# Optimization experiments

Hardware: AMD Instinct MI355X
Metric: run time of the kernel (lower is better)

Reference implementation:

```python
import jax, jax.numpy as jnp
import numpy as np

N = 50000        # nodes
F_IN = 128       # input features
HID = 128        # hidden_size
H = 4            # heads
C = HID // H     # per-head channels (32)
E_RAND = 800000  # random edges; + N self loops -> E = 850000
NEG_SLOPE = 0.2  # PyG GATConv default leaky_relu slope


def setup_inputs() -> dict:
    key = jax.random.key(0)
    ks = jax.random.split(key, 12)
    x = jax.random.normal(ks[0], (N, F_IN), jnp.float32)
    src_r = jax.random.randint(ks[1], (E_RAND,), 0, N)
    dst_r = jax.random.randint(ks[2], (E_RAND,), 0, N)
    loops = jnp.arange(N)
    src = jnp.concatenate([src_r, loops]).astype(jnp.int32)
    dst = jnp.concatenate([dst_r, loops]).astype(jnp.int32)

    def glorot(k, shape):
        fan_in, fan_out = shape[0], shape[-1]
        lim = np.sqrt(6.0 / (fan_in + fan_out)).astype(np.float32)
        return jax.random.uniform(k, shape, jnp.float32, -lim, lim)

    return {
        "x": x, "src": src, "dst": dst,
        "W0": glorot(ks[3], (F_IN, HID)),
        "a_src0": glorot(ks[4], (H, C)),
        "a_dst0": glorot(ks[5], (H, C)),
        "b0": jnp.zeros((HID,), jnp.float32),
        "W1": glorot(ks[6], (HID, HID)),
        "a_src1": glorot(ks[7], (H, C)),
        "a_dst1": glorot(ks[8], (H, C)),
        "b1": jnp.zeros((HID,), jnp.float32),
    }


def gat_layer(x, W, a_src, a_dst, b, src, dst):
    # linear projection -> [N, H, C]
    xp = (x @ W).reshape(-1, H, C)
    # per-node attention logits [N, H]
    al_src = jnp.einsum("nhc,hc->nh", xp, a_src)
    al_dst = jnp.einsum("nhc,hc->nh", xp, a_dst)
    # edge logits [E, H]
    e = jax.nn.leaky_relu(al_src[src] + al_dst[dst], NEG_SLOPE)
    # scatter softmax over incoming edges of each destination node
    m = jax.ops.segment_max(e, dst, num_segments=N)
    p = jnp.exp(e - m[dst])
    s = jax.ops.segment_sum(p, dst, num_segments=N)
    alpha = p / (s[dst] + 1e-16)
    # weighted message aggregation: [E, H, C] scatter-add -> [N, H, C]
    out = jax.ops.segment_sum(xp[src] * alpha[:, :, None], dst, num_segments=N)
    return out.reshape(-1, H * C) + b  # concat heads + bias


def reference(x, src, dst, W0, a_src0, a_dst0, b0, W1, a_src1, a_dst1, b1):
    h = jax.nn.relu(gat_layer(x, W0, a_src0, a_dst0, b0, src, dst))
    h = jax.nn.relu(gat_layer(h, W1, a_src1, a_dst1, b1, src, dst))
    return h
```

## Files before the change

### kernel.cpp

```cpp
#include <hip/hip_runtime.h>
#include <math.h>

#define NEG_SLOPE 0.2f
#define BCAP 4096
#define TILE 4096

using short8 = __attribute__((ext_vector_type(8))) short;
using f32x4 = __attribute__((ext_vector_type(4))) float;

__device__ __forceinline__ float leaky(float x) { return x > 0.f ? x : NEG_SLOPE * x; }

__device__ __forceinline__ float wmax64(float v) {
#pragma unroll
  for (int off = 32; off; off >>= 1) v = fmaxf(v, __shfl_xor(v, off));
  return v;
}
__device__ __forceinline__ float wsum64(float v) {
#pragma unroll
  for (int off = 32; off; off >>= 1) v += __shfl_xor(v, off);
  return v;
}

__device__ __forceinline__ unsigned short f2bf(float f) {
  union { float f; unsigned u; } x; x.f = f;
  unsigned r = x.u + 0x7fff + ((x.u >> 16) & 1);
  return (unsigned short)(r >> 16);
}
__device__ __forceinline__ float bf2f(unsigned short h) {
  union { unsigned u; float f; } x; x.u = (unsigned)h << 16;
  return x.f;
}

__device__ __forceinline__ void acc8(float* a, float p, uint4 rv) {
  a[0] += p * __uint_as_float(rv.x << 16);
  a[1] += p * __uint_as_float(rv.x & 0xffff0000u);
  a[2] += p * __uint_as_float(rv.y << 16);
  a[3] += p * __uint_as_float(rv.y & 0xffff0000u);
  a[4] += p * __uint_as_float(rv.z << 16);
  a[5] += p * __uint_as_float(rv.z & 0xffff0000u);
  a[6] += p * __uint_as_float(rv.w << 16);
  a[7] += p * __uint_as_float(rv.w & 0xffff0000u);
}

__global__ __launch_bounds__(256) void k_hist_wsplit(
    const int* __restrict__ dst, int* __restrict__ blkhist, int E, int nb, int nblk,
    const float* __restrict__ W0, const float* __restrict__ W1,
    unsigned short* __restrict__ Wth0, unsigned short* __restrict__ Wtl0,
    unsigned short* __restrict__ Wth1, unsigned short* __restrict__ Wtl1) {
  __shared__ int h[512];
  if (blockIdx.x < 128) {
    int i = blockIdx.x * 256 + threadIdx.x;
    int j = i & 16383;
    int k = j >> 7, n = j & 127;
    const float* W = (i < 16384) ? W0 : W1;
    float v = W[j];
    unsigned short hi = f2bf(v);
    unsigned short lo = f2bf(v - bf2f(hi));
    if (i < 16384) {
      Wth0[n * 128 + k] = hi;
      Wtl0[n * 128 + k] = lo;
    } else {
      Wth1[n * 128 + k] = hi;
      Wtl1[n * 128 + k] = lo;
    }
    return;
  }
  int blk = blockIdx.x - 128;
  for (int i = threadIdx.x; i < nb; i += 256) h[i] = 0;
  __syncthreads();
  int t0 = blk * TILE;
  int end = t0 + TILE < E ? t0 + TILE : E;
  for (int i = t0 + threadIdx.x; i < end; i += 256) atomicAdd(&h[dst[i] >> 7], 1);
  __syncthreads();
  for (int i = threadIdx.x; i < nb; i += 256) blkhist[(size_t)i * nblk + blk] = h[i];
}

__global__ __launch_bounds__(256) void k_bofs(int* __restrict__ blkhist,
                                              int* __restrict__ btot, int nblk) {
  __shared__ int sd[256];
  int b = blockIdx.x, t = threadIdx.x;
  int v = (t < nblk) ? blkhist[(size_t)b * nblk + t] : 0;
  sd[t] = v;
  __syncthreads();
  for (int off = 1; off < 256; off <<= 1) {
    int add = (t >= off) ? sd[t - off] : 0;
    __syncthreads();
    sd[t] += add;
    __syncthreads();
  }
  if (t < nblk) blkhist[(size_t)b * nblk + t] = sd[t] - v;
  if (t == 255) btot[b] = sd[255];
}

__global__ __launch_bounds__(256) void k_scatter2(
    const int* __restrict__ src, const int* __restrict__ dst,
    const int* __restrict__ blkhist, const int* __restrict__ btot,
    int2* __restrict__ bstore, int E, int nb, int nblk) {
  __shared__ int sd[256];
  __shared__ int bb[512];
  __shared__ int cur[512];
  int t = threadIdx.x, blk = blockIdx.x;
  int v0 = (2 * t < nb) ? btot[2 * t] : 0;
  int v1 = (2 * t + 1 < nb) ? btot[2 * t + 1] : 0;
  int s = v0 + v1;
  sd[t] = s;
  __syncthreads();
  for (int off = 1; off < 256; off <<= 1) {
    int add = (t >= off) ? sd[t - off] : 0;
    __syncthreads();
    sd[t] += add;
    __syncthreads();
  }
  int run = sd[t] - s;
  if (2 * t < nb) bb[2 * t] = run;
  if (2 * t + 1 < nb) bb[2 * t + 1] = run + v0;
  __syncthreads();
  for (int i = t; i < nb; i += 256)
    cur[i] = bb[i] + blkhist[(size_t)i * nblk + blk];
  __syncthreads();
  int t0 = blk * TILE;
  int end = t0 + TILE < E ? t0 + TILE : E;
  for (int i = t0 + t; i < end; i += 256) {
    int d = dst[i];
    int pos = atomicAdd(&cur[d >> 7], 1);
    bstore[pos] = make_int2(src[i], d);
  }
}

__global__ __launch_bounds__(256) void k_build(
    const int2* __restrict__ bstore, const int* __restrict__ btot,
    int* __restrict__ ssrc, int* __restrict__ deg, int* __restrict__ rstart, int N) {
  __shared__ int ls[BCAP];
  __shared__ unsigned char lloc[BCAP];
  __shared__ int lout[BCAP];
  __shared__ int hist[128];
  __shared__ int sc[128];
  __shared__ int lcur[128];
  __shared__ int red[256];
  int b = blockIdx.x;
  int t = threadIdx.x;
  int pacc = 0;
  for (int j = t; j < b; j += 256) pacc += btot[j];
  red[t] = pacc;
  __syncthreads();
  for (int off = 128; off; off >>= 1) {
    if (t < off) red[t] += red[t + off];
    __syncthreads();
  }
  int base = red[0];
  int cnt = btot[b];
  if (cnt > BCAP) cnt = BCAP;
  int nlo = b << 7;
  if (t < 128) { hist[t] = 0; lcur[t] = 0; }
  __syncthreads();
  for (int i = t; i < cnt; i += 256) {
    int2 e = bstore[base + i];
    int loc = e.y - nlo;
    ls[i] = e.x;
    lloc[i] = (unsigned char)loc;
    atomicAdd(&hist[loc], 1);
  }
  __syncthreads();
  int hv = (t < 128) ? hist[t] : 0;
  if (t < 128) sc[t] = hv;
  __syncthreads();
  for (int off = 1; off < 128; off <<= 1) {
    int add = (t < 128 && t >= off) ? sc[t - off] : 0;
    __syncthreads();
    if (t < 128) sc[t] += add;
    __syncthreads();
  }
  int lstart = (t < 128) ? sc[t] - hv : 0;
  if (t < 128) sc[t] = lstart;
  if (t < 128 && nlo + t < N) {
    deg[nlo + t] = hv;
    rstart[nlo + t] = base + lstart;
  }
  __syncthreads();
  for (int i = t; i < cnt; i += 256) {
    int loc = lloc[i];
    int slot = sc[loc] + atomicAdd(&lcur[loc], 1);
    lout[slot] = ls[i];
  }
  __syncthreads();
  for (int i = t; i < cnt; i += 256) ssrc[base + i] = lout[i];
}

#define PA 136
#define PW 40
__global__ __launch_bounds__(256, 2) void k_gemm_mfma(
    const float* __restrict__ A, const unsigned short* __restrict__ Wth,
    const unsigned short* __restrict__ Wtl, const float* __restrict__ a_src,
    const float* __restrict__ a_dst, unsigned short* __restrict__ xph,
    float* __restrict__ als, float* __restrict__ ald, int nrows) {
  __shared__ unsigned short Ah[64 * PA];
  __shared__ unsigned short Al[64 * PA];
  __shared__ unsigned short Wh[128 * PW];
  __shared__ unsigned short Wl[128 * PW];
  int t = threadIdx.x;
  int row0 = blockIdx.x * 64;

  const float4* A4 = (const float4*)A;
#pragma unroll
  for (int p = 0; p < 8; ++p) {
    int idx = t + p * 256;
    int row = idx >> 5, k4 = idx & 31;
    int gr = row0 + row;
    float4 v = make_float4(0.f, 0.f, 0.f, 0.f);
    if (gr < nrows) v = A4[(size_t)gr * 32 + k4];
    ushort4 hi, lo;
    hi.x = f2bf(v.x); lo.x = f2bf(v.x - bf2f(hi.x));
    hi.y = f2bf(v.y); lo.y = f2bf(v.y - bf2f(hi.y));
    hi.z = f2bf(v.z); lo.z = f2bf(v.z - bf2f(hi.z));
    hi.w = f2bf(v.w); lo.w = f2bf(v.w - bf2f(hi.w));
    *(ushort4*)&Ah[row * PA + k4 * 4] = hi;
    *(ushort4*)&Al[row * PA + k4 * 4] = lo;
  }

  int lane = t & 63, wv = t >> 6;
  int wr = wv >> 1, wc = wv & 1;
  int ml = lane & 15, q = lane >> 4;
  f32x4 acc[2][4] = {};

  for (int kb = 0; kb < 4; ++kb) {
    __syncthreads();
    int k0 = kb * 32;
#pragma unroll
    for (int p = 0; p < 8; ++p) {
      int idx = t + p * 256;
      int n = idx >> 4, kp = idx & 15;
      *(unsigned*)&Wh[n * PW + kp * 2] =
          *(const unsigned*)(Wth + (size_t)n * 128 + k0 + kp * 2);
      *(unsigned*)&Wl[n * PW + kp * 2] =
          *(const unsigned*)(Wtl + (size_t)n * 128 + k0 + kp * 2);
    }
    __syncthreads();
    int kf = k0 + q * 8;
    short8 a_h0 = *(const short8*)&Ah[(wr * 32 + ml) * PA + kf];
    short8 a_h1 = *(const short8*)&Ah[(wr * 32 + 16 + ml) * PA + kf];
    short8 a_l0 = *(const short8*)&Al[(wr * 32 + ml) * PA + kf];
    short8 a_l1 = *(const short8*)&Al[(wr * 32 + 16 + ml) * PA + kf];
#pragma unroll
    for (int ct = 0; ct < 4; ++ct) {
      int nb = (wc * 64 + ct * 16 + ml) * PW + q * 8;
      short8 b_h = *(const short8*)&Wh[nb];
      short8 b_l = *(const short8*)&Wl[nb];
      acc[0][ct] = __builtin_amdgcn_mfma_f32_16x16x32_bf16(a_h0, b_h, acc[0][ct], 0, 0, 0);
      acc[0][ct] = __builtin_amdgcn_mfma_f32_16x16x32_bf16(a_h0, b_l, acc[0][ct], 0, 0, 0);
      acc[0][ct] = __builtin_amdgcn_mfma_f32_16x16x32_bf16(a_l0, b_h, acc[0][ct], 0, 0, 0);
      acc[1][ct] = __builtin_amdgcn_mfma_f32_16x16x32_bf16(a_h1, b_h, acc[1][ct], 0, 0, 0);
      acc[1][ct] = __builtin_amdgcn_mfma_f32_16x16x32_bf16(a_h1, b_l, acc[1][ct], 0, 0, 0);
      acc[1][ct] = __builtin_amdgcn_mfma_f32_16x16x32_bf16(a_l1, b_h, acc[1][ct], 0, 0, 0);
    }
  }

  float asr[4], adr[4];
#pragma unroll
  for (int ct = 0; ct < 4; ++ct) {
    int col = (wc * 2 + (ct >> 1)) * 32 + (ct & 1) * 16 + ml;
    asr[ct] = a_src[col];
    adr[ct] = a_dst[col];
  }

#pragma unroll
  for (int rt = 0; rt < 2; ++rt) {
#pragma unroll
    for (int r = 0; r < 4; ++r) {
      int gr = row0 + wr * 32 + rt * 16 + q * 4 + r;
      bool valid = gr < nrows;
      if (valid) {
#pragma unroll
        for (int ct = 0; ct < 4; ++ct) {
          int gc = wc * 64 + ct * 16 + ml;
          xph[(size_t)gr * 128 + gc] = f2bf(acc[rt][ct][r]);
        }
      }
      float p0 = acc[rt][0][r] * asr[0] + acc[rt][1][r] * asr[1];
      float p1 = acc[rt][2][r] * asr[2] + acc[rt][3][r] * asr[3];
      float d0 = acc[rt][0][r] * adr[0] + acc[rt][1][r] * adr[1];
      float d1 = acc[rt][2][r] * adr[2] + acc[rt][3][r] * adr[3];
#pragma unroll
      for (int off = 1; off <= 8; off <<= 1) {
        p0 += __shfl_xor(p0, off); p1 += __shfl_xor(p1, off);
        d0 += __shfl_xor(d0, off); d1 += __shfl_xor(d1, off);
      }
      if (ml == 0 && valid) {
        als[(size_t)gr * 4 + wc * 2] = p0;
        als[(size_t)gr * 4 + wc * 2 + 1] = p1;
        ald[(size_t)gr * 4 + wc * 2] = d0;
        ald[(size_t)gr * 4 + wc * 2 + 1] = d1;
      }
    }
  }
}

__global__ __launch_bounds__(256) void k_aggregate(
    const unsigned short* __restrict__ xph, const float* __restrict__ als,
    const float* __restrict__ ald, const int* __restrict__ rstart,
    const int* __restrict__ deg, const int* __restrict__ ssrc,
    const float* __restrict__ bias, float* __restrict__ out, int N) {
  __shared__ float pbuf[4][128 * 4];
  __shared__ int snbuf[4][128];
  int wv = threadIdx.x >> 6;
  int lane = threadIdx.x & 63;
  int n = (blockIdx.x * blockDim.x + threadIdx.x) >> 6;
  if (n >= N) return;
  int start = rstart[n];
  int d = deg[n];
  float4 adv = *(const float4*)(ald + (size_t)n * 4);

  float m0, m1, m2, m3;
  float s0 = 0.f, s1 = 0.f, s2 = 0.f, s3 = 0.f;
  if (d <= 64) {
    int i = lane;
    bool valid = i < d;
    int sn = valid ? ssrc[start + i] : 0;
    if (valid) snbuf[wv][i] = sn;
    float4 av = *(const float4*)(als + (size_t)sn * 4);
    float L0 = valid ? leaky(av.x + adv.x) : -INFINITY;
    float L1 = valid ? leaky(av.y + adv.y) : -INFINITY;
    float L2 = valid ? leaky(av.z + adv.z) : -INFINITY;
    float L3 = valid ? leaky(av.w + adv.w) : -INFINITY;
    m0 = wmax64(L0); m1 = wmax64(L1); m2 = wmax64(L2); m3 = wmax64(L3);
    float p0 = __expf(L0 - m0);
    float p1 = __expf(L1 - m1);
    float p2 = __expf(L2 - m2);
    float p3 = __expf(L3 - m3);
    *(float4*)&pbuf[wv][lane * 4] = make_float4(p0, p1, p2, p3);
    s0 = wsum64(p0); s1 = wsum64(p1); s2 = wsum64(p2); s3 = wsum64(p3);
  } else {
    m0 = m1 = m2 = m3 = -INFINITY;
    for (int base = 0; base < d; base += 64) {
      int i = base + lane;
      bool valid = i < d;
      int sn = valid ? ssrc[start + i] : 0;
      if (valid) snbuf[wv][i] = sn;
      float4 av = *(const float4*)(als + (size_t)sn * 4);
      float L0 = valid ? leaky(av.x + adv.x) : -INFINITY;
      float L1 = valid ? leaky(av.y + adv.y) : -INFINITY;
      float L2 = valid ? leaky(av.z + adv.z) : -INFINITY;
      float L3 = valid ? leaky(av.w + adv.w) : -INFINITY;
      if (valid) *(float4*)&pbuf[wv][i * 4] = make_float4(L0, L1, L2, L3);
      m0 = fmaxf(m0, wmax64(L0)); m1 = fmaxf(m1, wmax64(L1));
      m2 = fmaxf(m2, wmax64(L2)); m3 = fmaxf(m3, wmax64(L3));
    }
    for (int base = 0; base < d; base += 64) {
      int i = base + lane;
      bool valid = i < d;
      float4 lv = valid ? *(const float4*)&pbuf[wv][i * 4]
                        : make_float4(-INFINITY, -INFINITY, -INFINITY, -INFINITY);
      float p0 = __expf(lv.x - m0), p1 = __expf(lv.y - m1);
      float p2 = __expf(lv.z - m2), p3 = __expf(lv.w - m3);
      if (valid) *(float4*)&pbuf[wv][i * 4] = make_float4(p0, p1, p2, p3);
      s0 += wsum64(p0); s1 += wsum64(p1); s2 += wsum64(p2); s3 += wsum64(p3);
    }
  }

  int cg = lane & 15;
  int es = lane >> 4;
  int c0 = cg * 8;
  int h = cg >> 2;
  float a[8] = {0.f, 0.f, 0.f, 0.f, 0.f, 0.f, 0.f, 0.f};
  int t = es;
  for (; t + 12 < d; t += 16) {
    int sn0 = snbuf[wv][t];
    int sn1 = snbuf[wv][t + 4];
    int sn2 = snbuf[wv][t + 8];
    int sn3 = snbuf[wv][t + 12];
    float q0 = pbuf[wv][t * 4 + h];
    float q1 = pbuf[wv][(t + 4) * 4 + h];
    float q2 = pbuf[wv][(t + 8) * 4 + h];
    float q3 = pbuf[wv][(t + 12) * 4 + h];
    uint4 r0 = *(const uint4*)(xph + (size_t)sn0 * 128 + c0);
    uint4 r1 = *(const uint4*)(xph + (size_t)sn1 * 128 + c0);
    uint4 r2 = *(const uint4*)(xph + (size_t)sn2 * 128 + c0);
    uint4 r3 = *(const uint4*)(xph + (size_t)sn3 * 128 + c0);
    acc8(a, q0, r0);
    acc8(a, q1, r1);
    acc8(a, q2, r2);
    acc8(a, q3, r3);
  }
  for (; t < d; t += 4) {
    int sn = snbuf[wv][t];
    float p = pbuf[wv][t * 4 + h];
    uint4 rv = *(const uint4*)(xph + (size_t)sn * 128 + c0);
    acc8(a, p, rv);
  }
#pragma unroll
  for (int off = 16; off <= 32; off <<= 1) {
#pragma unroll
    for (int j = 0; j < 8; ++j) a[j] += __shfl_xor(a[j], off);
  }
  if (es == 0) {
    float sden = h == 0 ? s0 : h == 1 ? s1 : h == 2 ? s2 : s3;
    float inv = 1.f / (sden + 1e-16f);
    float4 bv0 = *(const float4*)(bias + c0);
    float4 bv1 = *(const float4*)(bias + c0 + 4);
    float4 o0, o1;
    o0.x = fmaxf(a[0] * inv + bv0.x, 0.f);
    o0.y = fmaxf(a[1] * inv + bv0.y, 0.f);
    o0.z = fmaxf(a[2] * inv + bv0.z, 0.f);
    o0.w = fmaxf(a[3] * inv + bv0.w, 0.f);
    o1.x = fmaxf(a[4] * inv + bv1.x, 0.f);
    o1.y = fmaxf(a[5] * inv + bv1.y, 0.f);
    o1.z = fmaxf(a[6] * inv + bv1.z, 0.f);
    o1.w = fmaxf(a[7] * inv + bv1.w, 0.f);
    *(float4*)(out + (size_t)n * 128 + c0) = o0;
    *(float4*)(out + (size_t)n * 128 + c0 + 4) = o1;
  }
}

extern "C" void kernel_launch(void* const* d_in, const int* in_sizes, int n_in,
                              void* d_out, int out_size, void* d_ws, size_t ws_size,
                              hipStream_t stream) {
  const float* x   = (const float*)d_in[0];
  const int*   src = (const int*)d_in[1];
  const int*   dst = (const int*)d_in[2];
  const float* W0  = (const float*)d_in[3];
  const float* as0 = (const float*)d_in[4];
  const float* ad0 = (const float*)d_in[5];
  const float* b0  = (const float*)d_in[6];
  const float* W1  = (const float*)d_in[7];
  const float* as1 = (const float*)d_in[8];
  const float* ad1 = (const float*)d_in[9];
  const float* b1  = (const float*)d_in[10];
  float* out = (float*)d_out;

  int N = in_sizes[0] / 128;
  int E = in_sizes[1];
  int NB = (N + 127) >> 7;
  int NBLK = (E + TILE - 1) / TILE;

  char* w = (char*)d_ws;
  auto alloc = [&](size_t bytes) {
    char* p = w;
    w += (bytes + 255) & ~(size_t)255;
    return p;
  };
  int* deg     = (int*)alloc((size_t)N * 4);
  int* rstart  = (int*)alloc((size_t)N * 4);
  int* blkhist = (int*)alloc((size_t)NB * NBLK * 4);
  int* btot    = (int*)alloc((size_t)NB * 4);
  int2* bstore = (int2*)alloc((size_t)E * 8);
  int* ssrc    = (int*)alloc((size_t)E * 4);
  unsigned short* xph = (unsigned short*)alloc((size_t)N * 128 * 2);
  float* hbuf  = (float*)alloc((size_t)N * 128 * 4);
  float* als   = (float*)alloc((size_t)N * 4 * 4);
  float* ald   = (float*)alloc((size_t)N * 4 * 4);
  unsigned short* Wth0 = (unsigned short*)alloc(16384 * 2);
  unsigned short* Wtl0 = (unsigned short*)alloc(16384 * 2);
  unsigned short* Wth1 = (unsigned short*)alloc(16384 * 2);
  unsigned short* Wtl1 = (unsigned short*)alloc(16384 * 2);

  k_hist_wsplit<<<128 + NBLK, 256, 0, stream>>>(dst, blkhist, E, NB, NBLK,
                                                W0, W1, Wth0, Wtl0, Wth1, Wtl1);
  k_bofs<<<NB, 256, 0, stream>>>(blkhist, btot, NBLK);
  k_scatter2<<<NBLK, 256, 0, stream>>>(src, dst, blkhist, btot, bstore, E, NB, NBLK);
  k_build<<<NB, 256, 0, stream>>>(bstore, btot, ssrc, deg, rstart, N);

  int gb = (N + 63) / 64;
  k_gemm_mfma<<<gb, 256, 0, stream>>>(x, Wth0, Wtl0, as0, ad0, xph, als, ald, N);
  k_aggregate<<<(N + 3) / 4, 256, 0, stream>>>(xph, als, ald, rstart, deg, ssrc, b0, hbuf, N);

  k_gemm_mfma<<<gb, 256, 0, stream>>>(hbuf, Wth1, Wtl1, as1, ad1, xph, als, ald, N);
  k_aggregate<<<(N + 3) / 4, 256, 0, stream>>>(xph, als, ald, rstart, deg, ssrc, b1, out, N);
}
```

Measured before the change: 249.9 us.

## Fuse layer-0 GEMM into scatter kernel, pack bucket entries, simplify gather loop

Layer-0 GEMM blocks are appended to the scatter kernel's grid, so the projection runs alongside the edge bucketing and one launch is removed. Bucket entries are packed into a single int (local dst in the high 16 bits, src in the low 16), which halves the bucket store traffic. TILE doubles to 8192, halving the number of scatter blocks. The aggregation loop's manual 4-way unroll is replaced by a plain loop with unroll 2, giving up some memory-level parallelism in exchange for lower register pressure. The 16-bit src packing is only valid while N is at most 65536.

```diff
diff --git a/kernel.cpp b/kernel.cpp
--- a/kernel.cpp
+++ b/kernel.cpp
@@ -3,7 +3,7 @@
 
 #define NEG_SLOPE 0.2f
 #define BCAP 4096
-#define TILE 4096
+#define TILE 8192
 
 using short8 = __attribute__((ext_vector_type(8))) short;
 using f32x4 = __attribute__((ext_vector_type(4))) float;
@@ -40,6 +40,114 @@
   a[5] += p * __uint_as_float(rv.z & 0xffff0000u);
   a[6] += p * __uint_as_float(rv.w << 16);
   a[7] += p * __uint_as_float(rv.w & 0xffff0000u);
+}
+
+#define PA 136
+#define PW 40
+__device__ void gemm_body(
+    const float* __restrict__ A, const unsigned short* __restrict__ Wth,
+    const unsigned short* __restrict__ Wtl, const float* __restrict__ a_src,
+    const float* __restrict__ a_dst, unsigned short* __restrict__ xph,
+    float* __restrict__ als, float* __restrict__ ald, int nrows, int blk) {
+  __shared__ unsigned short Ah[64 * PA];
+  __shared__ unsigned short Al[64 * PA];
+  __shared__ unsigned short Wh[128 * PW];
+  __shared__ unsigned short Wl[128 * PW];
+  int t = threadIdx.x;
+  int row0 = blk * 64;
+
+  const float4* A4 = (const float4*)A;
+#pragma unroll
+  for (int p = 0; p < 8; ++p) {
+    int idx = t + p * 256;
+    int row = idx >> 5, k4 = idx & 31;
+    int gr = row0 + row;
+    float4 v = make_float4(0.f, 0.f, 0.f, 0.f);
+    if (gr < nrows) v = A4[(size_t)gr * 32 + k4];
+    ushort4 hi, lo;
+    hi.x = f2bf(v.x); lo.x = f2bf(v.x - bf2f(hi.x));
+    hi.y = f2bf(v.y); lo.y = f2bf(v.y - bf2f(hi.y));
+    hi.z = f2bf(v.z); lo.z = f2bf(v.z - bf2f(hi.z));
+    hi.w = f2bf(v.w); lo.w = f2bf(v.w - bf2f(hi.w));
+    *(ushort4*)&Ah[row * PA + k4 * 4] = hi;
+    *(ushort4*)&Al[row * PA + k4 * 4] = lo;
+  }
+
+  int lane = t & 63, wv = t >> 6;
+  int wr = wv >> 1, wc = wv & 1;
+  int ml = lane & 15, q = lane >> 4;
+  f32x4 acc[2][4] = {};
+
+  for (int kb = 0; kb < 4; ++kb) {
+    __syncthreads();
+    int k0 = kb * 32;
+#pragma unroll
+    for (int p = 0; p < 8; ++p) {
+      int idx = t + p * 256;
+      int n = idx >> 4, kp = idx & 15;
+      *(unsigned*)&Wh[n * PW + kp * 2] =
+          *(const unsigned*)(Wth + (size_t)n * 128 + k0 + kp * 2);
+      *(unsigned*)&Wl[n * PW + kp * 2] =
+          *(const unsigned*)(Wtl + (size_t)n * 128 + k0 + kp * 2);
+    }
+    __syncthreads();
+    int kf = k0 + q * 8;
+    short8 a_h0 = *(const short8*)&Ah[(wr * 32 + ml) * PA + kf];
+    short8 a_h1 = *(const short8*)&Ah[(wr * 32 + 16 + ml) * PA + kf];
+    short8 a_l0 = *(const short8*)&Al[(wr * 32 + ml) * PA + kf];
+    short8 a_l1 = *(const short8*)&Al[(wr * 32 + 16 + ml) * PA + kf];
+#pragma unroll
+    for (int ct = 0; ct < 4; ++ct) {
+      int nb = (wc * 64 + ct * 16 + ml) * PW + q * 8;
+      short8 b_h = *(const short8*)&Wh[nb];
+      short8 b_l = *(const short8*)&Wl[nb];
+      acc[0][ct] = __builtin_amdgcn_mfma_f32_16x16x32_bf16(a_h0, b_h, acc[0][ct], 0, 0, 0);
+      acc[0][ct] = __builtin_amdgcn_mfma_f32_16x16x32_bf16(a_h0, b_l, acc[0][ct], 0, 0, 0);
+      acc[0][ct] = __builtin_amdgcn_mfma_f32_16x16x32_bf16(a_l0, b_h, acc[0][ct], 0, 0, 0);
+      acc[1][ct] = __builtin_amdgcn_mfma_f32_16x16x32_bf16(a_h1, b_h, acc[1][ct], 0, 0, 0);
+      acc[1][ct] = __builtin_amdgcn_mfma_f32_16x16x32_bf16(a_h1, b_l, acc[1][ct], 0, 0, 0);
+      acc[1][ct] = __builtin_amdgcn_mfma_f32_16x16x32_bf16(a_l1, b_h, acc[1][ct], 0, 0, 0);
+    }
+  }
+
+  float asr[4], adr[4];
+#pragma unroll
+  for (int ct = 0; ct < 4; ++ct) {
+    int col = (wc * 2 + (ct >> 1)) * 32 + (ct & 1) * 16 + ml;
+    asr[ct] = a_src[col];
+    adr[ct] = a_dst[col];
+  }
+
+#pragma unroll
+  for (int rt = 0; rt < 2; ++rt) {
+#pragma unroll
+    for (int r = 0; r < 4; ++r) {
+      int gr = row0 + wr * 32 + rt * 16 + q * 4 + r;
+      bool valid = gr < nrows;
+      if (valid) {
+#pragma unroll
+        for (int ct = 0; ct < 4; ++ct) {
+          int gc = wc * 64 + ct * 16 + ml;
+          xph[(size_t)gr * 128 + gc] = f2bf(acc[rt][ct][r]);
+        }
+      }
+      float p0 = acc[rt][0][r] * asr[0] + acc[rt][1][r] * asr[1];
+      float p1 = acc[rt][2][r] * asr[2] + acc[rt][3][r] * asr[3];
+      float d0 = acc[rt][0][r] * adr[0] + acc[rt][1][r] * adr[1];
+      float d1 = acc[rt][2][r] * adr[2] + acc[rt][3][r] * adr[3];
+#pragma unroll
+      for (int off = 1; off <= 8; off <<= 1) {
+        p0 += __shfl_xor(p0, off); p1 += __shfl_xor(p1, off);
+        d0 += __shfl_xor(d0, off); d1 += __shfl_xor(d1, off);
+      }
+      if (ml == 0 && valid) {
+        als[(size_t)gr * 4 + wc * 2] = p0;
+        als[(size_t)gr * 4 + wc * 2 + 1] = p1;
+        ald[(size_t)gr * 4 + wc * 2] = d0;
+        ald[(size_t)gr * 4 + wc * 2 + 1] = d1;
+      }
+    }
+  }
 }
 
 __global__ __launch_bounds__(256) void k_hist_wsplit(
@@ -92,10 +200,18 @@
   if (t == 255) btot[b] = sd[255];
 }
 
-__global__ __launch_bounds__(256) void k_scatter2(
+__global__ __launch_bounds__(256, 2) void k_scatter2_gemm(
     const int* __restrict__ src, const int* __restrict__ dst,
     const int* __restrict__ blkhist, const int* __restrict__ btot,
-    int2* __restrict__ bstore, int E, int nb, int nblk) {
+    int* __restrict__ bstore, int E, int nb, int nblk,
+    const float* __restrict__ A, const unsigned short* __restrict__ Wth,
+    const unsigned short* __restrict__ Wtl, const float* __restrict__ a_src,
+    const float* __restrict__ a_dst, unsigned short* __restrict__ xph,
+    float* __restrict__ als, float* __restrict__ ald, int nrows) {
+  if ((int)blockIdx.x >= nblk) {
+    gemm_body(A, Wth, Wtl, a_src, a_dst, xph, als, ald, nrows, blockIdx.x - nblk);
+    return;
+  }
   __shared__ int sd[256];
   __shared__ int bb[512];
   __shared__ int cur[512];
@@ -123,12 +239,12 @@
   for (int i = t0 + t; i < end; i += 256) {
     int d = dst[i];
     int pos = atomicAdd(&cur[d >> 7], 1);
-    bstore[pos] = make_int2(src[i], d);
+    bstore[pos] = ((d & 127) << 16) | src[i];
   }
 }
 
 __global__ __launch_bounds__(256) void k_build(
-    const int2* __restrict__ bstore, const int* __restrict__ btot,
+    const int* __restrict__ bstore, const int* __restrict__ btot,
     int* __restrict__ ssrc, int* __restrict__ deg, int* __restrict__ rstart, int N) {
   __shared__ int ls[BCAP];
   __shared__ unsigned char lloc[BCAP];
@@ -154,9 +270,9 @@
   if (t < 128) { hist[t] = 0; lcur[t] = 0; }
   __syncthreads();
   for (int i = t; i < cnt; i += 256) {
-    int2 e = bstore[base + i];
-    int loc = e.y - nlo;
-    ls[i] = e.x;
+    int e = bstore[base + i];
+    int loc = e >> 16;
+    ls[i] = e & 0xffff;
     lloc[i] = (unsigned char)loc;
     atomicAdd(&hist[loc], 1);
   }
@@ -186,112 +302,12 @@
   for (int i = t; i < cnt; i += 256) ssrc[base + i] = lout[i];
 }
 
-#define PA 136
-#define PW 40
 __global__ __launch_bounds__(256, 2) void k_gemm_mfma(
     const float* __restrict__ A, const unsigned short* __restrict__ Wth,
     const unsigned short* __restrict__ Wtl, const float* __restrict__ a_src,
     const float* __restrict__ a_dst, unsigned short* __restrict__ xph,
     float* __restrict__ als, float* __restrict__ ald, int nrows) {
-  __shared__ unsigned short Ah[64 * PA];
-  __shared__ unsigned short Al[64 * PA];
-  __shared__ unsigned short Wh[128 * PW];
-  __shared__ unsigned short Wl[128 * PW];
-  int t = threadIdx.x;
-  int row0 = blockIdx.x * 64;
-
-  const float4* A4 = (const float4*)A;
-#pragma unroll
-  for (int p = 0; p < 8; ++p) {
-    int idx = t + p * 256;
-    int row = idx >> 5, k4 = idx & 31;
-    int gr = row0 + row;
-    float4 v = make_float4(0.f, 0.f, 0.f, 0.f);
-    if (gr < nrows) v = A4[(size_t)gr * 32 + k4];
-    ushort4 hi, lo;
-    hi.x = f2bf(v.x); lo.x = f2bf(v.x - bf2f(hi.x));
-    hi.y = f2bf(v.y); lo.y = f2bf(v.y - bf2f(hi.y));
-    hi.z = f2bf(v.z); lo.z = f2bf(v.z - bf2f(hi.z));
-    hi.w = f2bf(v.w); lo.w = f2bf(v.w - bf2f(hi.w));
-    *(ushort4*)&Ah[row * PA + k4 * 4] = hi;
-    *(ushort4*)&Al[row * PA + k4 * 4] = lo;
-  }
-
-  int lane = t & 63, wv = t >> 6;
-  int wr = wv >> 1, wc = wv & 1;
-  int ml = lane & 15, q = lane >> 4;
-  f32x4 acc[2][4] = {};
-
-  for (int kb = 0; kb < 4; ++kb) {
-    __syncthreads();
-    int k0 = kb * 32;
-#pragma unroll
-    for (int p = 0; p < 8; ++p) {
-      int idx = t + p * 256;
-      int n = idx >> 4, kp = idx & 15;
-      *(unsigned*)&Wh[n * PW + kp * 2] =
-          *(const unsigned*)(Wth + (size_t)n * 128 + k0 + kp * 2);
-      *(unsigned*)&Wl[n * PW + kp * 2] =
-          *(const unsigned*)(Wtl + (size_t)n * 128 + k0 + kp * 2);
-    }
-    __syncthreads();
-    int kf = k0 + q * 8;
-    short8 a_h0 = *(const short8*)&Ah[(wr * 32 + ml) * PA + kf];
-    short8 a_h1 = *(const short8*)&Ah[(wr * 32 + 16 + ml) * PA + kf];
-    short8 a_l0 = *(const short8*)&Al[(wr * 32 + ml) * PA + kf];
-    short8 a_l1 = *(const short8*)&Al[(wr * 32 + 16 + ml) * PA + kf];
-#pragma unroll
-    for (int ct = 0; ct < 4; ++ct) {
-      int nb = (wc * 64 + ct * 16 + ml) * PW + q * 8;
-      short8 b_h = *(const short8*)&Wh[nb];
-      short8 b_l = *(const short8*)&Wl[nb];
-      acc[0][ct] = __builtin_amdgcn_mfma_f32_16x16x32_bf16(a_h0, b_h, acc[0][ct], 0, 0, 0);
-      acc[0][ct] = __builtin_amdgcn_mfma_f32_16x16x32_bf16(a_h0, b_l, acc[0][ct], 0, 0, 0);
-      acc[0][ct] = __builtin_amdgcn_mfma_f32_16x16x32_bf16(a_l0, b_h, acc[0][ct], 0, 0, 0);
-      acc[1][ct] = __builtin_amdgcn_mfma_f32_16x16x32_bf16(a_h1, b_h, acc[1][ct], 0, 0, 0);
-      acc[1][ct] = __builtin_amdgcn_mfma_f32_16x16x32_bf16(a_h1, b_l, acc[1][ct], 0, 0, 0);
-      acc[1][ct] = __builtin_amdgcn_mfma_f32_16x16x32_bf16(a_l1, b_h, acc[1][ct], 0, 0, 0);
-    }
-  }
-
-  float asr[4], adr[4];
-#pragma unroll
-  for (int ct = 0; ct < 4; ++ct) {
-    int col = (wc * 2 + (ct >> 1)) * 32 + (ct & 1) * 16 + ml;
-    asr[ct] = a_src[col];
-    adr[ct] = a_dst[col];
-  }
-
-#pragma unroll
-  for (int rt = 0; rt < 2; ++rt) {
-#pragma unroll
-    for (int r = 0; r < 4; ++r) {
-      int gr = row0 + wr * 32 + rt * 16 + q * 4 + r;
-      bool valid = gr < nrows;
-      if (valid) {
-#pragma unroll
-        for (int ct = 0; ct < 4; ++ct) {
-          int gc = wc * 64 + ct * 16 + ml;
-          xph[(size_t)gr * 128 + gc] = f2bf(acc[rt][ct][r]);
-        }
-      }
-      float p0 = acc[rt][0][r] * asr[0] + acc[rt][1][r] * asr[1];
-      float p1 = acc[rt][2][r] * asr[2] + acc[rt][3][r] * asr[3];
-      float d0 = acc[rt][0][r] * adr[0] + acc[rt][1][r] * adr[1];
-      float d1 = acc[rt][2][r] * adr[2] + acc[rt][3][r] * adr[3];
-#pragma unroll
-      for (int off = 1; off <= 8; off <<= 1) {
-        p0 += __shfl_xor(p0, off); p1 += __shfl_xor(p1, off);
-        d0 += __shfl_xor(d0, off); d1 += __shfl_xor(d1, off);
-      }
-      if (ml == 0 && valid) {
-        als[(size_t)gr * 4 + wc * 2] = p0;
-        als[(size_t)gr * 4 + wc * 2 + 1] = p1;
-        ald[(size_t)gr * 4 + wc * 2] = d0;
-        ald[(size_t)gr * 4 + wc * 2 + 1] = d1;
-      }
-    }
-  }
+  gemm_body(A, Wth, Wtl, a_src, a_dst, xph, als, ald, nrows, blockIdx.x);
 }
 
 __global__ __launch_bounds__(256) void k_aggregate(
@@ -361,26 +377,8 @@
   int c0 = cg * 8;
   int h = cg >> 2;
   float a[8] = {0.f, 0.f, 0.f, 0.f, 0.f, 0.f, 0.f, 0.f};
-  int t = es;
-  for (; t + 12 < d; t += 16) {
-    int sn0 = snbuf[wv][t];
-    int sn1 = snbuf[wv][t + 4];
-    int sn2 = snbuf[wv][t + 8];
-    int sn3 = snbuf[wv][t + 12];
-    float q0 = pbuf[wv][t * 4 + h];
-    float q1 = pbuf[wv][(t + 4) * 4 + h];
-    float q2 = pbuf[wv][(t + 8) * 4 + h];
-    float q3 = pbuf[wv][(t + 12) * 4 + h];
-    uint4 r0 = *(const uint4*)(xph + (size_t)sn0 * 128 + c0);
-    uint4 r1 = *(const uint4*)(xph + (size_t)sn1 * 128 + c0);
-    uint4 r2 = *(const uint4*)(xph + (size_t)sn2 * 128 + c0);
-    uint4 r3 = *(const uint4*)(xph + (size_t)sn3 * 128 + c0);
-    acc8(a, q0, r0);
-    acc8(a, q1, r1);
-    acc8(a, q2, r2);
-    acc8(a, q3, r3);
-  }
-  for (; t < d; t += 4) {
+#pragma unroll 2
+  for (int t = es; t < d; t += 4) {
     int sn = snbuf[wv][t];
     float p = pbuf[wv][t * 4 + h];
     uint4 rv = *(const uint4*)(xph + (size_t)sn * 128 + c0);
@@ -441,7 +439,7 @@
   int* rstart  = (int*)alloc((size_t)N * 4);
   int* blkhist = (int*)alloc((size_t)NB * NBLK * 4);
   int* btot    = (int*)alloc((size_t)NB * 4);
-  int2* bstore = (int2*)alloc((size_t)E * 8);
+  int* bstore  = (int*)alloc((size_t)E * 4);
   int* ssrc    = (int*)alloc((size_t)E * 4);
   unsigned short* xph = (unsigned short*)alloc((size_t)N * 128 * 2);
   float* hbuf  = (float*)alloc((size_t)N * 128 * 4);
@@ -452,16 +450,16 @@
   unsigned short* Wth1 = (unsigned short*)alloc(16384 * 2);
   unsigned short* Wtl1 = (unsigned short*)alloc(16384 * 2);
 
+  int gb = (N + 63) / 64;
+
   k_hist_wsplit<<<128 + NBLK, 256, 0, stream>>>(dst, blkhist, E, NB, NBLK,
                                                 W0, W1, Wth0, Wtl0, Wth1, Wtl1);
   k_bofs<<<NB, 256, 0, stream>>>(blkhist, btot, NBLK);
-  k_scatter2<<<NBLK, 256, 0, stream>>>(src, dst, blkhist, btot, bstore, E, NB, NBLK);
+  k_scatter2_gemm<<<NBLK + gb, 256, 0, stream>>>(
+      src, dst, blkhist, btot, bstore, E, NB, NBLK,
+      x, Wth0, Wtl0, as0, ad0, xph, als, ald, N);
   k_build<<<NB, 256, 0, stream>>>(bstore, btot, ssrc, deg, rstart, N);
-
-  int gb = (N + 63) / 64;
-  k_gemm_mfma<<<gb, 256, 0, stream>>>(x, Wth0, Wtl0, as0, ad0, xph, als, ald, N);
   k_aggregate<<<(N + 3) / 4, 256, 0, stream>>>(xph, als, ald, rstart, deg, ssrc, b0, hbuf, N);
-
   k_gemm_mfma<<<gb, 256, 0, stream>>>(hbuf, Wth1, Wtl1, as1, ad1, xph, als, ald, N);
   k_aggregate<<<(N + 3) / 4, 256, 0, stream>>>(xph, als, ald, rstart, deg, ssrc, b1, out, N);
 }
```

After: 247.1 us. No clear change (-1.1%).
